# Kernel optimization log

Hardware: AMD Instinct MI355X
Metric: run time of the kernel (lower is better)

Reference implementation:

```python
import jax, jax.numpy as jnp
from jax import lax
import numpy as np


def _rnn_tanh_layer(x, W_ih, W_hh, b_ih, b_hh, return_seq):
    # x: [B, T, I]; W_ih: [H, I]; W_hh: [H, H]
    B = x.shape[0]
    H = W_hh.shape[0]
    # Precompute input projection for all timesteps (one big GEMM).
    xw = jnp.einsum('bti,hi->bth', x, W_ih) + b_ih + b_hh  # [B, T, H]
    xw_t = jnp.swapaxes(xw, 0, 1)  # [T, B, H] for scan
    h0 = jnp.zeros((B, H), dtype=x.dtype)

    def step(h, xt):
        h_new = jnp.tanh(xt + h @ W_hh.T)
        return h_new, (h_new if return_seq else None)

    hT, hs = lax.scan(step, h0, xw_t)
    if return_seq:
        return jnp.swapaxes(hs, 0, 1), hT  # [B, T, H], [B, H]
    return None, hT


def setup_inputs() -> dict:
    key = jax.random.key(0)
    ks = jax.random.split(key, 12)
    B, T, I, H1, H2, C = 512, 1024, 32, 128, 64, 10

    def unif(k, shape, fan):
        bound = 1.0 / np.sqrt(fan)
        return jax.random.uniform(k, shape, jnp.float32, -bound, bound)

    return {
        'x': jax.random.normal(ks[0], (B, T, I), jnp.float32),
        'W_ih1': unif(ks[1], (H1, I), H1),
        'W_hh1': unif(ks[2], (H1, H1), H1),
        'b_ih1': unif(ks[3], (H1,), H1),
        'b_hh1': unif(ks[4], (H1,), H1),
        'W_ih2': unif(ks[5], (H2, H1), H2),
        'W_hh2': unif(ks[6], (H2, H2), H2),
        'b_ih2': unif(ks[7], (H2,), H2),
        'b_hh2': unif(ks[8], (H2,), H2),
        'W_fc': unif(ks[9], (C, H2), H2),
        'b_fc': unif(ks[10], (C,), H2),
    }


def reference(x, W_ih1, W_hh1, b_ih1, b_hh1, W_ih2, W_hh2, b_ih2, b_hh2, W_fc, b_fc):
    out1, _h1 = _rnn_tanh_layer(x, W_ih1, W_hh1, b_ih1, b_hh1, return_seq=True)
    _none, h2 = _rnn_tanh_layer(out1, W_ih2, W_hh2, b_ih2, b_hh2, return_seq=False)
    # Dropout(p=0.3) is identity in eval mode.
    logits = h2 @ W_fc.T + b_fc  # [B, 10]
    return logits
```

## Files before the change

### kernel.cpp

```cpp
#include <hip/hip_runtime.h>
#include <stdint.h>


typedef _Float16 f16x8 __attribute__((ext_vector_type(8)));
typedef _Float16 f16x4 __attribute__((ext_vector_type(4)));
typedef float f32x4 __attribute__((ext_vector_type(4)));

#define MFMA_F16(A, B, C) __builtin_amdgcn_mfma_f32_16x16x32_f16((A), (B), (C), 0, 0, 0)

__device__ __forceinline__ float tanh_fast(float x) {
  float t = __builtin_amdgcn_exp2f(x * 2.88539008177792681472f);
  return 1.0f - 2.0f * __builtin_amdgcn_rcpf(t + 1.0f);
}

__device__ __forceinline__ uint32_t pk16(float a, float b) {
  return __builtin_bit_cast(uint32_t, __builtin_amdgcn_cvt_pkrtz(a, b));
}

__device__ __forceinline__ void sync_lds() {
  asm volatile("s_waitcnt lgkmcnt(0)\n\ts_barrier" ::: "memory");
}

__device__ __forceinline__ f16x8 cvt8w(const float* s) {
  f32x4 a = *(const f32x4*)s;
  f32x4 b = *(const f32x4*)(s + 4);
  f16x8 r;
#pragma unroll
  for (int j = 0; j < 4; ++j) { r[j] = (_Float16)a[j]; r[4 + j] = (_Float16)b[j]; }
  return r;
}

__device__ __forceinline__ f16x8 pack_x8(const f32x4& a, const f32x4& b) {
  union { uint32_t u[4]; f16x8 v; } tmp;
  tmp.u[0] = pk16(a[0], a[1]); tmp.u[1] = pk16(a[2], a[3]);
  tmp.u[2] = pk16(b[0], b[1]); tmp.u[3] = pk16(b[2], b[3]);
  return tmp.v;
}

__global__ __launch_bounds__(256) void xw_pre(
    const float* __restrict__ x, const float* __restrict__ Wih1,
    const float* __restrict__ bih1, const float* __restrict__ bhh1,
    uint2* __restrict__ xw)
{
  const int tid  = threadIdx.x;
  const int w    = tid >> 6, lane = tid & 63;
  const int g    = lane >> 4, n = lane & 15;
  const int gb   = blockIdx.x >> 3;
  const int t0   = ((blockIdx.x & 7) << 7) + (w << 5);

  f16x8 aI[8];
  f32x4 bias[8];
#pragma unroll
  for (int m = 0; m < 8; ++m) {
    aI[m] = cvt8w(Wih1 + (m * 16 + n) * 32 + g * 8);
#pragma unroll
    for (int r = 0; r < 4; ++r)
      bias[m][r] = bih1[m * 16 + g * 4 + r] + bhh1[m * 16 + g * 4 + r];
  }

  const float* xp = x + ((size_t)(gb * 16 + n) * 1024 + t0) * 32 + g * 8;
  uint2* xo = xw + (size_t)(gb * 1024 + t0) * 512 + lane;

  f32x4 xa = *(const f32x4*)(xp);
  f32x4 xb = *(const f32x4*)(xp + 4);
  for (int tt = 0; tt < 32; ++tt) {
    f32x4 na, nb;
    if (tt < 31) {
      na = *(const f32x4*)(xp + (tt + 1) * 32);
      nb = *(const f32x4*)(xp + (tt + 1) * 32 + 4);
    }
    f16x8 xf = pack_x8(xa, xb);
#pragma unroll
    for (int m = 0; m < 8; ++m) {
      f32x4 d = MFMA_F16(aI[m], xf, bias[m]);
      xo[tt * 512 + m * 64] = make_uint2(pk16(d[0], d[1]), pk16(d[2], d[3]));
    }
    xa = na; xb = nb;
  }
}

__global__ __attribute__((amdgpu_waves_per_eu(2, 2))) __launch_bounds__(512)
void rnn_rec(
    const float* __restrict__ Whh1,
    const float* __restrict__ Wih2, const float* __restrict__ Whh2,
    const float* __restrict__ bih2, const float* __restrict__ bhh2,
    const float* __restrict__ Wfc,  const float* __restrict__ bfc,
    const uint2* __restrict__ xw,
    float* __restrict__ out)
{
  constexpr int T = 1024, H1 = 128, H2 = 64, BB = 16;
  constexpr int H1_0 = 0,     H1_1 = 4096;
  constexpr int H2_0 = 8192,  H2_1 = 10240;
  constexpr int PB_0 = 12288, PB_1 = 16384;
  constexpr int H2F  = 20480;
  __shared__ __align__(16) unsigned char smem[24576];

  const int tid  = threadIdx.x;
  const int w    = tid >> 6;
  const int lane = tid & 63;
  const int g    = lane >> 4;
  const int n    = lane & 15;
  const int b0   = blockIdx.x * BB;

  {
    uint32_t* p = (uint32_t*)smem;
    for (int i = tid; i < 1024; i += 512) p[i] = 0u;
    uint32_t* q = (uint32_t*)(smem + H2_0);
    for (int i = tid; i < 1024; i += 512) q[i] = 0u;
  }

  auto tanh_pack = [&](const f32x4& a, uint32_t& lo, uint32_t& hi) {
    lo = pk16(tanh_fast(a[0]), tanh_fast(a[1]));
    hi = pk16(tanh_fast(a[2]), tanh_fast(a[3]));
  };

  __syncthreads();

  const f32x4 zero = {0.f, 0.f, 0.f, 0.f};
  const int lb = lane * 16;

  if (w < 4) {
    f16x8 aU[2][4], aI2[4];
    f32x4 bias2v;
#pragma unroll
    for (int ti = 0; ti < 2; ++ti) {
      const int ch = (2 * w + ti) * 16 + n;
#pragma unroll
      for (int k4 = 0; k4 < 4; ++k4)
        aU[ti][k4] = cvt8w(Whh1 + ch * H1 + k4 * 32 + g * 8);
    }
#pragma unroll
    for (int k4 = 0; k4 < 4; ++k4)
      aI2[k4] = cvt8w(Wih2 + (16 * w + n) * H1 + k4 * 32 + g * 8);
#pragma unroll
    for (int r = 0; r < 4; ++r)
      bias2v[r] = bih2[16 * w + g * 4 + r] + bhh2[16 * w + g * 4 + r];

    int woff[2];
#pragma unroll
    for (int ti = 0; ti < 2; ++ti)
      woff[ti] = w * 1024 + (2 * ti + (g >> 1)) * 256 + n * 16 + (g & 1) * 8;
    const int pw_rel = w * 1024 + lb;

    const uint2* xwp = xw + (size_t)blockIdx.x * T * 512 + lane;
    const int ti0 = (2 * w) * 64, ti1 = (2 * w + 1) * 64;

    auto cvtC = [](uint2 v) -> f32x4 {
      f16x4 h = __builtin_bit_cast(f16x4, v);
      f32x4 r;
#pragma unroll
      for (int i = 0; i < 4; ++i) r[i] = (float)h[i];
      return r;
    };

    uint2 qA0 = xwp[0 * 512 + ti0], qA1 = xwp[0 * 512 + ti1];
    uint2 qB0 = xwp[1 * 512 + ti0], qB1 = xwp[1 * 512 + ti1];

    auto stepL1 = [&](int t, int cur, uint2& s0, uint2& s1) {
      const char* H1c = (const char*)smem + (cur ? H1_1 : H1_0);
      char*       H1n = (char*)smem + (cur ? H1_0 : H1_1);
      char*       Pw  = (char*)smem + (cur ? PB_1 : PB_0);
      f16x8 b1k0 = *(const f16x8*)(H1c + 0 * 1024 + lb);
      f16x8 b1k1 = *(const f16x8*)(H1c + 1 * 1024 + lb);
      f16x8 b1k2 = *(const f16x8*)(H1c + 2 * 1024 + lb);
      f16x8 b1k3 = *(const f16x8*)(H1c + 3 * 1024 + lb);
      f32x4 accI0 = cvtC(s0), accI1 = cvtC(s1);
      if (t + 2 < T) {
        s0 = xwp[(t + 2) * 512 + ti0];
        s1 = xwp[(t + 2) * 512 + ti1];
      }
      f32x4 aA0 = MFMA_F16(aU[0][0], b1k0, accI0);
      f32x4 aB0 = MFMA_F16(aU[0][2], b1k2, zero);
      f32x4 aA1 = MFMA_F16(aU[1][0], b1k0, accI1);
      f32x4 aB1 = MFMA_F16(aU[1][2], b1k2, zero);
      aA0 = MFMA_F16(aU[0][1], b1k1, aA0);
      aB0 = MFMA_F16(aU[0][3], b1k3, aB0);
      aA1 = MFMA_F16(aU[1][1], b1k1, aA1);
      aB1 = MFMA_F16(aU[1][3], b1k3, aB1);
      {
        f32x4 cA = MFMA_F16(aI2[0], b1k0, bias2v);
        f32x4 cB = MFMA_F16(aI2[1], b1k1, zero);
        cA = MFMA_F16(aI2[2], b1k2, cA);
        cB = MFMA_F16(aI2[3], b1k3, cB);
        *(f32x4*)(Pw + pw_rel) = cA + cB;
      }
      {
        f32x4 s0v = aA0 + aB0;
        uint32_t lo, hi;
        tanh_pack(s0v, lo, hi);
        *(uint2*)(H1n + woff[0]) = make_uint2(lo, hi);
      }
      {
        f32x4 s1v = aA1 + aB1;
        uint32_t lo, hi;
        tanh_pack(s1v, lo, hi);
        *(uint2*)(H1n + woff[1]) = make_uint2(lo, hi);
      }
      sync_lds();
    };

    for (int t = 0; t < T; t += 2) {
      stepL1(t + 0, 0, qA0, qA1);
      stepL1(t + 1, 1, qB0, qB1);
    }
    {
      const char* H1c = (const char*)smem + H1_0;
      f16x8 b1k0 = *(const f16x8*)(H1c + 0 * 1024 + lb);
      f16x8 b1k1 = *(const f16x8*)(H1c + 1 * 1024 + lb);
      f16x8 b1k2 = *(const f16x8*)(H1c + 2 * 1024 + lb);
      f16x8 b1k3 = *(const f16x8*)(H1c + 3 * 1024 + lb);
      f32x4 cA = MFMA_F16(aI2[0], b1k0, bias2v);
      f32x4 cB = MFMA_F16(aI2[1], b1k1, zero);
      cA = MFMA_F16(aI2[2], b1k2, cA);
      cB = MFMA_F16(aI2[3], b1k3, cB);
      *(f32x4*)((char*)smem + PB_0 + pw_rel) = cA + cB;
    }
    sync_lds();
    sync_lds();
  } else {
    const int j2 = w - 4;
    f16x8 aR2[2];
#pragma unroll
    for (int k2 = 0; k2 < 2; ++k2)
      aR2[k2] = cvt8w(Whh2 + (16 * j2 + n) * H2 + k2 * 32 + g * 8);

    const int h2w = (j2 >> 1) * 1024 + (2 * (j2 & 1) + (g >> 1)) * 256
                  + n * 16 + (g & 1) * 8;
    const int proff = j2 * 1024 + lb;

    auto stepL2 = [&](int s, int cur) {
      if (s > 1) {
        const char* Pr  = (const char*)smem + (cur ? PB_0 : PB_1);
        const char* H2r = (const char*)smem + (cur ? H2_1 : H2_0);
        char*       H2w = (char*)smem + (cur ? H2_0 : H2_1);
        f32x4 part = *(const f32x4*)(Pr + proff);
        f16x8 b2k0 = *(const f16x8*)(H2r + 0 * 1024 + lb);
        f16x8 b2k1 = *(const f16x8*)(H2r + 1 * 1024 + lb);
        f32x4 z2 = MFMA_F16(aR2[0], b2k0, part);
        z2 = MFMA_F16(aR2[1], b2k1, z2);
        uint32_t lo, hi;
        tanh_pack(z2, lo, hi);
        *(uint2*)(H2w + h2w) = make_uint2(lo, hi);
      }
      sync_lds();
    };

    for (int s = 0; s < T; s += 2) {
      stepL2(s + 0, 0);
      stepL2(s + 1, 1);
    }
    {
      const char* Pr  = (const char*)smem + PB_1;
      const char* H2r = (const char*)smem + H2_0;
      char*       H2w = (char*)smem + H2_1;
      f32x4 part = *(const f32x4*)(Pr + proff);
      f16x8 b2k0 = *(const f16x8*)(H2r + 0 * 1024 + lb);
      f16x8 b2k1 = *(const f16x8*)(H2r + 1 * 1024 + lb);
      f32x4 z2 = MFMA_F16(aR2[0], b2k0, part);
      z2 = MFMA_F16(aR2[1], b2k1, z2);
      uint32_t lo, hi;
      tanh_pack(z2, lo, hi);
      *(uint2*)(H2w + h2w) = make_uint2(lo, hi);
    }
    sync_lds();
    {
      const char* Pr  = (const char*)smem + PB_0;
      const char* H2r = (const char*)smem + H2_1;
      f32x4 part = *(const f32x4*)(Pr + proff);
      f16x8 b2k0 = *(const f16x8*)(H2r + 0 * 1024 + lb);
      f16x8 b2k1 = *(const f16x8*)(H2r + 1 * 1024 + lb);
      f32x4 z2 = MFMA_F16(aR2[0], b2k0, part);
      z2 = MFMA_F16(aR2[1], b2k1, z2);
      f32x4 hv;
#pragma unroll
      for (int r = 0; r < 4; ++r) hv[r] = tanh_fast(z2[r]);
      *(f32x4*)(smem + H2F + n * 256 + (16 * j2 + 4 * g) * 4) = hv;
    }
    sync_lds();
  }

  if (tid < BB * 10) {
    const int b = tid / 10, c = tid % 10;
    const float* hrow = (const float*)(smem + H2F + b * 256);
    float acc = bfc[c];
#pragma unroll 8
    for (int k = 0; k < 64; ++k) acc += hrow[k] * Wfc[c * 64 + k];
    out[(size_t)(b0 + b) * 10 + c] = acc;
  }
}

__global__ __launch_bounds__(512) void rnn_fallback(
    const float* __restrict__ x,
    const float* __restrict__ Wih1, const float* __restrict__ Whh1,
    const float* __restrict__ bih1, const float* __restrict__ bhh1,
    const float* __restrict__ Wih2, const float* __restrict__ Whh2,
    const float* __restrict__ bih2, const float* __restrict__ bhh2,
    const float* __restrict__ Wfc,  const float* __restrict__ bfc,
    float* __restrict__ out)
{
  constexpr int T = 1024, I = 32, H1 = 128, H2 = 64, BB = 16;
  constexpr int R1 = 272, R2 = 144;
  constexpr int H1_0 = 0, H1_1 = 4352;
  constexpr int H2_0 = 8704, H2_1 = 11008;
  constexpr int H2F  = 13312;
  __shared__ __align__(16) unsigned char smem[17408];
  const int tid = threadIdx.x, w = tid >> 6, lane = tid & 63;
  const int g = lane >> 4, n = lane & 15, b0 = blockIdx.x * BB;
  {
    uint32_t* p = (uint32_t*)smem;
    for (int i = tid; i < 1088; i += 512) p[i] = 0u;
    uint32_t* q = (uint32_t*)(smem + H2_0);
    for (int i = tid; i < 576; i += 512) q[i] = 0u;
  }
  int roff1[4];
#pragma unroll
  for (int k4 = 0; k4 < 4; ++k4) roff1[k4] = n * R1 + k4 * 64 + g * 16;
  auto tanh_pack = [&](const f32x4& a, uint32_t& lo, uint32_t& hi) {
    lo = pk16(tanh_fast(a[0]), tanh_fast(a[1]));
    hi = pk16(tanh_fast(a[2]), tanh_fast(a[3]));
  };
  __syncthreads();
  const f32x4 zero = {0.f, 0.f, 0.f, 0.f};
  if (w < 4) {
    f16x8 aU[2][4], aI1[2];
    f32x4 bias1[2];
#pragma unroll
    for (int ti = 0; ti < 2; ++ti) {
      const int ch = (2 * w + ti) * 16 + n;
#pragma unroll
      for (int k4 = 0; k4 < 4; ++k4)
        aU[ti][k4] = cvt8w(Whh1 + ch * H1 + k4 * 32 + g * 8);
      aI1[ti] = cvt8w(Wih1 + ch * I + g * 8);
      const int cb = (2 * w + ti) * 16 + g * 4;
#pragma unroll
      for (int r = 0; r < 4; ++r) bias1[ti][r] = bih1[cb + r] + bhh1[cb + r];
    }
    int woff[2];
#pragma unroll
    for (int ti = 0; ti < 2; ++ti)
      woff[ti] = n * R1 + (2 * w + ti) * 32 + g * 8;
    const float* xp = x + (size_t)(b0 + n) * T * I + g * 8;
    f32x4 qa = *(const f32x4*)(xp), qb = *(const f32x4*)(xp + 4);
    f32x4 accI0, accI1;
    {
      f16x8 xf = pack_x8(qa, qb);
      accI0 = MFMA_F16(aI1[0], xf, bias1[0]);
      accI1 = MFMA_F16(aI1[1], xf, bias1[1]);
    }
    for (int t = 0; t < T; ++t) {
      const int cur = t & 1;
      const char* H1c = (const char*)smem + (cur ? H1_1 : H1_0);
      char*       H1n = (char*)smem + (cur ? H1_0 : H1_1);
      f16x8 b1k0 = *(const f16x8*)(H1c + roff1[0]);
      f16x8 b1k1 = *(const f16x8*)(H1c + roff1[1]);
      f16x8 b1k2 = *(const f16x8*)(H1c + roff1[2]);
      f16x8 b1k3 = *(const f16x8*)(H1c + roff1[3]);
      if (t + 1 < T) {
        qa = *(const f32x4*)(xp + (t + 1) * I);
        qb = *(const f32x4*)(xp + (t + 1) * I + 4);
      }
      f32x4 aA0 = MFMA_F16(aU[0][0], b1k0, accI0);
      f32x4 aB0 = MFMA_F16(aU[0][2], b1k2, zero);
      f32x4 aA1 = MFMA_F16(aU[1][0], b1k0, accI1);
      f32x4 aB1 = MFMA_F16(aU[1][2], b1k2, zero);
      aA0 = MFMA_F16(aU[0][1], b1k1, aA0);
      aB0 = MFMA_F16(aU[0][3], b1k3, aB0);
      aA1 = MFMA_F16(aU[1][1], b1k1, aA1);
      aB1 = MFMA_F16(aU[1][3], b1k3, aB1);
      if (t + 1 < T) {
        f16x8 xf = pack_x8(qa, qb);
        accI0 = MFMA_F16(aI1[0], xf, bias1[0]);
        accI1 = MFMA_F16(aI1[1], xf, bias1[1]);
      }
      uint32_t lo, hi;
      f32x4 s0 = aA0 + aB0;
      tanh_pack(s0, lo, hi);
      *(uint2*)(H1n + woff[0]) = make_uint2(lo, hi);
      f32x4 s1 = aA1 + aB1;
      tanh_pack(s1, lo, hi);
      *(uint2*)(H1n + woff[1]) = make_uint2(lo, hi);
      sync_lds();
    }
  } else {
    const int j = w - 4;
    f16x8 aI2[4], aR2[2];
#pragma unroll
    for (int k4 = 0; k4 < 4; ++k4)
      aI2[k4] = cvt8w(Wih2 + (16 * j + n) * H1 + k4 * 32 + g * 8);
#pragma unroll
    for (int k2 = 0; k2 < 2; ++k2)
      aR2[k2] = cvt8w(Whh2 + (16 * j + n) * H2 + k2 * 32 + g * 8);
    f32x4 bias2;
#pragma unroll
    for (int r = 0; r < 4; ++r)
      bias2[r] = bih2[16 * j + g * 4 + r] + bhh2[16 * j + g * 4 + r];
    int roff2[2];
#pragma unroll
    for (int k2 = 0; k2 < 2; ++k2) roff2[k2] = n * R2 + k2 * 64 + g * 16;
    const int woff2 = n * R2 + j * 32 + g * 8;
    auto l2_body = [&](const char* H1c, const char* H2r, f32x4& s) {
      f16x8 b1k0 = *(const f16x8*)(H1c + roff1[0]);
      f16x8 b1k1 = *(const f16x8*)(H1c + roff1[1]);
      f16x8 b1k2 = *(const f16x8*)(H1c + roff1[2]);
      f16x8 b1k3 = *(const f16x8*)(H1c + roff1[3]);
      f16x8 b2k0 = *(const f16x8*)(H2r + roff2[0]);
      f16x8 b2k1 = *(const f16x8*)(H2r + roff2[1]);
      f32x4 cA = MFMA_F16(aI2[0], b1k0, bias2);
      f32x4 cB = MFMA_F16(aI2[1], b1k1, zero);
      f32x4 cC = MFMA_F16(aR2[0], b2k0, zero);
      cA = MFMA_F16(aI2[2], b1k2, cA);
      cB = MFMA_F16(aI2[3], b1k3, cB);
      cC = MFMA_F16(aR2[1], b2k1, cC);
      s = cA + cB + cC;
    };
    for (int t = 0; t < T; ++t) {
      const int cur = t & 1;
      if (t > 0) {
        const char* H1c = (const char*)smem + (cur ? H1_1 : H1_0);
        const char* H2r = (const char*)smem + (cur ? H2_0 : H2_1);
        char*       H2w = (char*)smem + (cur ? H2_1 : H2_0);
        f32x4 s;
        l2_body(H1c, H2r, s);
        uint32_t lo, hi;
        tanh_pack(s, lo, hi);
        *(uint2*)(H2w + woff2) = make_uint2(lo, hi);
      }
      sync_lds();
    }
    {
      f32x4 s;
      l2_body((const char*)smem + H1_0, (const char*)smem + H2_1, s);
      f32x4 hv;
#pragma unroll
      for (int r = 0; r < 4; ++r) hv[r] = tanh_fast(s[r]);
      *(f32x4*)(smem + H2F + n * 256 + (16 * j + 4 * g) * 4) = hv;
    }
  }
  sync_lds();
  if (tid < BB * 10) {
    const int b = tid / 10, c = tid % 10;
    const float* hrow = (const float*)(smem + H2F + b * 256);
    float acc = bfc[c];
#pragma unroll 8
    for (int k = 0; k < 64; ++k) acc += hrow[k] * Wfc[c * 64 + k];
    out[(size_t)(b0 + b) * 10 + c] = acc;
  }
}

extern "C" void kernel_launch(void* const* d_in, const int* in_sizes, int n_in,
                              void* d_out, int out_size, void* d_ws, size_t ws_size,
                              hipStream_t stream) {
  const float* x    = (const float*)d_in[0];
  const float* Wih1 = (const float*)d_in[1];
  const float* Whh1 = (const float*)d_in[2];
  const float* bih1 = (const float*)d_in[3];
  const float* bhh1 = (const float*)d_in[4];
  const float* Wih2 = (const float*)d_in[5];
  const float* Whh2 = (const float*)d_in[6];
  const float* bih2 = (const float*)d_in[7];
  const float* bhh2 = (const float*)d_in[8];
  const float* Wfc  = (const float*)d_in[9];
  const float* bfc  = (const float*)d_in[10];

  const size_t xw_bytes = (size_t)512 * 1024 * 128 * 2;
  if (ws_size >= xw_bytes) {
    uint2* xw = (uint2*)d_ws;
    hipLaunchKernelGGL(xw_pre, dim3(256), dim3(256), 0, stream,
                       x, Wih1, bih1, bhh1, xw);
    hipLaunchKernelGGL(rnn_rec, dim3(512 / 16), dim3(512), 0, stream,
                       Whh1, Wih2, Whh2, bih2, bhh2, Wfc, bfc,
                       (const uint2*)xw, (float*)d_out);
  } else {
    hipLaunchKernelGGL(rnn_fallback, dim3(512 / 16), dim3(512), 0, stream,
                       x, Wih1, Whh1, bih1, bhh1, Wih2, Whh2, bih2, bhh2,
                       Wfc, bfc, (float*)d_out);
  }
}
```

Baseline: 495.7 us.

## Move layer-2 input projection into layer-2 waves, drop partial-sum LDS buffer

Moves the layer-2 input projection (Wih2·h1) off the layer-1 waves and onto the layer-2 waves, which now read h1 straight from the shared ping-pong buffer. This removes the fp32 partial-sum staging buffers in LDS and shortens the layer-2 pipeline lag from two steps to one. Layer-1 waves each step now do only their recurrent MFMAs, shortening the critical path between barriers. In exchange the layer-2 waves do six MFMAs per step instead of two and load four more fragments, which could become the slower side of each barrier.

```diff
diff --git a/kernel.cpp b/kernel.cpp
--- a/kernel.cpp
+++ b/kernel.cpp
@@ -89,11 +89,10 @@
     float* __restrict__ out)
 {
   constexpr int T = 1024, H1 = 128, H2 = 64, BB = 16;
-  constexpr int H1_0 = 0,     H1_1 = 4096;
-  constexpr int H2_0 = 8192,  H2_1 = 10240;
-  constexpr int PB_0 = 12288, PB_1 = 16384;
-  constexpr int H2F  = 20480;
-  __shared__ __align__(16) unsigned char smem[24576];
+  constexpr int H1_0 = 0,    H1_1 = 4096;
+  constexpr int H2_0 = 8192, H2_1 = 10240;
+  constexpr int H2F  = 12288;
+  __shared__ __align__(16) unsigned char smem[16384];
 
   const int tid  = threadIdx.x;
   const int w    = tid >> 6;
@@ -106,7 +105,7 @@
     uint32_t* p = (uint32_t*)smem;
     for (int i = tid; i < 1024; i += 512) p[i] = 0u;
     uint32_t* q = (uint32_t*)(smem + H2_0);
-    for (int i = tid; i < 1024; i += 512) q[i] = 0u;
+    for (int i = tid; i < 512; i += 512) q[i] = 0u;
   }
 
   auto tanh_pack = [&](const f32x4& a, uint32_t& lo, uint32_t& hi) {
@@ -120,8 +119,7 @@
   const int lb = lane * 16;
 
   if (w < 4) {
-    f16x8 aU[2][4], aI2[4];
-    f32x4 bias2v;
+    f16x8 aU[2][4];
 #pragma unroll
     for (int ti = 0; ti < 2; ++ti) {
       const int ch = (2 * w + ti) * 16 + n;
@@ -129,18 +127,10 @@
       for (int k4 = 0; k4 < 4; ++k4)
         aU[ti][k4] = cvt8w(Whh1 + ch * H1 + k4 * 32 + g * 8);
     }
-#pragma unroll
-    for (int k4 = 0; k4 < 4; ++k4)
-      aI2[k4] = cvt8w(Wih2 + (16 * w + n) * H1 + k4 * 32 + g * 8);
-#pragma unroll
-    for (int r = 0; r < 4; ++r)
-      bias2v[r] = bih2[16 * w + g * 4 + r] + bhh2[16 * w + g * 4 + r];
-
     int woff[2];
 #pragma unroll
     for (int ti = 0; ti < 2; ++ti)
       woff[ti] = w * 1024 + (2 * ti + (g >> 1)) * 256 + n * 16 + (g & 1) * 8;
-    const int pw_rel = w * 1024 + lb;
 
     const uint2* xwp = xw + (size_t)blockIdx.x * T * 512 + lane;
     const int ti0 = (2 * w) * 64, ti1 = (2 * w + 1) * 64;
@@ -159,7 +149,6 @@
     auto stepL1 = [&](int t, int cur, uint2& s0, uint2& s1) {
       const char* H1c = (const char*)smem + (cur ? H1_1 : H1_0);
       char*       H1n = (char*)smem + (cur ? H1_0 : H1_1);
-      char*       Pw  = (char*)smem + (cur ? PB_1 : PB_0);
       f16x8 b1k0 = *(const f16x8*)(H1c + 0 * 1024 + lb);
       f16x8 b1k1 = *(const f16x8*)(H1c + 1 * 1024 + lb);
       f16x8 b1k2 = *(const f16x8*)(H1c + 2 * 1024 + lb);
@@ -178,13 +167,6 @@
       aA1 = MFMA_F16(aU[1][1], b1k1, aA1);
       aB1 = MFMA_F16(aU[1][3], b1k3, aB1);
       {
-        f32x4 cA = MFMA_F16(aI2[0], b1k0, bias2v);
-        f32x4 cB = MFMA_F16(aI2[1], b1k1, zero);
-        cA = MFMA_F16(aI2[2], b1k2, cA);
-        cB = MFMA_F16(aI2[3], b1k3, cB);
-        *(f32x4*)(Pw + pw_rel) = cA + cB;
-      }
-      {
         f32x4 s0v = aA0 + aB0;
         uint32_t lo, hi;
         tanh_pack(s0v, lo, hi);
@@ -203,81 +185,69 @@
       stepL1(t + 0, 0, qA0, qA1);
       stepL1(t + 1, 1, qB0, qB1);
     }
-    {
-      const char* H1c = (const char*)smem + H1_0;
+  } else {
+    const int j = w - 4;
+    f16x8 aI2[4], aR2[2];
+#pragma unroll
+    for (int k4 = 0; k4 < 4; ++k4)
+      aI2[k4] = cvt8w(Wih2 + (16 * j + n) * H1 + k4 * 32 + g * 8);
+#pragma unroll
+    for (int k2 = 0; k2 < 2; ++k2)
+      aR2[k2] = cvt8w(Whh2 + (16 * j + n) * H2 + k2 * 32 + g * 8);
+    f32x4 bias2;
+#pragma unroll
+    for (int r = 0; r < 4; ++r)
+      bias2[r] = bih2[16 * j + g * 4 + r] + bhh2[16 * j + g * 4 + r];
+
+    const int h2w = (j >> 1) * 1024 + (2 * (j & 1) + (g >> 1)) * 256
+                  + n * 16 + (g & 1) * 8;
+
+    auto l2_body = [&](const char* H1c, const char* H2r, f32x4& s) {
       f16x8 b1k0 = *(const f16x8*)(H1c + 0 * 1024 + lb);
       f16x8 b1k1 = *(const f16x8*)(H1c + 1 * 1024 + lb);
       f16x8 b1k2 = *(const f16x8*)(H1c + 2 * 1024 + lb);
       f16x8 b1k3 = *(const f16x8*)(H1c + 3 * 1024 + lb);
-      f32x4 cA = MFMA_F16(aI2[0], b1k0, bias2v);
+      f16x8 b2k0 = *(const f16x8*)(H2r + 0 * 1024 + lb);
+      f16x8 b2k1 = *(const f16x8*)(H2r + 1 * 1024 + lb);
+      f32x4 cA = MFMA_F16(aI2[0], b1k0, bias2);
       f32x4 cB = MFMA_F16(aI2[1], b1k1, zero);
+      f32x4 cC = MFMA_F16(aR2[0], b2k0, zero);
       cA = MFMA_F16(aI2[2], b1k2, cA);
       cB = MFMA_F16(aI2[3], b1k3, cB);
-      *(f32x4*)((char*)smem + PB_0 + pw_rel) = cA + cB;
-    }
-    sync_lds();
-    sync_lds();
-  } else {
-    const int j2 = w - 4;
-    f16x8 aR2[2];
-#pragma unroll
-    for (int k2 = 0; k2 < 2; ++k2)
-      aR2[k2] = cvt8w(Whh2 + (16 * j2 + n) * H2 + k2 * 32 + g * 8);
-
-    const int h2w = (j2 >> 1) * 1024 + (2 * (j2 & 1) + (g >> 1)) * 256
-                  + n * 16 + (g & 1) * 8;
-    const int proff = j2 * 1024 + lb;
-
-    auto stepL2 = [&](int s, int cur) {
-      if (s > 1) {
-        const char* Pr  = (const char*)smem + (cur ? PB_0 : PB_1);
-        const char* H2r = (const char*)smem + (cur ? H2_1 : H2_0);
-        char*       H2w = (char*)smem + (cur ? H2_0 : H2_1);
-        f32x4 part = *(const f32x4*)(Pr + proff);
-        f16x8 b2k0 = *(const f16x8*)(H2r + 0 * 1024 + lb);
-        f16x8 b2k1 = *(const f16x8*)(H2r + 1 * 1024 + lb);
-        f32x4 z2 = MFMA_F16(aR2[0], b2k0, part);
-        z2 = MFMA_F16(aR2[1], b2k1, z2);
+      cC = MFMA_F16(aR2[1], b2k1, cC);
+      s = cA + cB + cC;
+    };
+
+    auto stepL2 = [&](int t, int cur) {
+      if (t > 0) {
+        const char* H1c = (const char*)smem + (cur ? H1_1 : H1_0);
+        const char* H2r = (const char*)smem + (cur ? H2_0 : H2_1);
+        char*       H2w = (char*)smem + (cur ? H2_1 : H2_0);
+        f32x4 s;
+        l2_body(H1c, H2r, s);
         uint32_t lo, hi;
-        tanh_pack(z2, lo, hi);
+        tanh_pack(s, lo, hi);
         *(uint2*)(H2w + h2w) = make_uint2(lo, hi);
       }
       sync_lds();
     };
 
-    for (int s = 0; s < T; s += 2) {
-      stepL2(s + 0, 0);
-      stepL2(s + 1, 1);
-    }
+    for (int t = 0; t < T; t += 2) {
+      stepL2(t + 0, 0);
+      stepL2(t + 1, 1);
+    }
+
     {
-      const char* Pr  = (const char*)smem + PB_1;
-      const char* H2r = (const char*)smem + H2_0;
-      char*       H2w = (char*)smem + H2_1;
-      f32x4 part = *(const f32x4*)(Pr + proff);
-      f16x8 b2k0 = *(const f16x8*)(H2r + 0 * 1024 + lb);
-      f16x8 b2k1 = *(const f16x8*)(H2r + 1 * 1024 + lb);
-      f32x4 z2 = MFMA_F16(aR2[0], b2k0, part);
-      z2 = MFMA_F16(aR2[1], b2k1, z2);
-      uint32_t lo, hi;
-      tanh_pack(z2, lo, hi);
-      *(uint2*)(H2w + h2w) = make_uint2(lo, hi);
-    }
-    sync_lds();
-    {
-      const char* Pr  = (const char*)smem + PB_0;
-      const char* H2r = (const char*)smem + H2_1;
-      f32x4 part = *(const f32x4*)(Pr + proff);
-      f16x8 b2k0 = *(const f16x8*)(H2r + 0 * 1024 + lb);
-      f16x8 b2k1 = *(const f16x8*)(H2r + 1 * 1024 + lb);
-      f32x4 z2 = MFMA_F16(aR2[0], b2k0, part);
-      z2 = MFMA_F16(aR2[1], b2k1, z2);
+      f32x4 s;
+      l2_body((const char*)smem + H1_0, (const char*)smem + H2_1, s);
       f32x4 hv;
 #pragma unroll
-      for (int r = 0; r < 4; ++r) hv[r] = tanh_fast(z2[r]);
-      *(f32x4*)(smem + H2F + n * 256 + (16 * j2 + 4 * g) * 4) = hv;
-    }
-    sync_lds();
-  }
+      for (int r = 0; r < 4; ++r) hv[r] = tanh_fast(s[r]);
+      *(f32x4*)(smem + H2F + n * 256 + (16 * j + 4 * g) * 4) = hv;
+    }
+  }
+
+  sync_lds();
 
   if (tid < BB * 10) {
     const int b = tid / 10, c = tid % 10;
```

Measured after the change: 426.3 us (median of 2 runs). 14.0% less time.
